# Kernel optimization log

Hardware: AMD Instinct MI355X
Metric: run time of the kernel (lower is better)

## Reference

```python
import jax, jax.numpy as jnp
import numpy as np

FPS_RATIO = 0.1
K = 20
EPS = 1e-6
COS_EPS = 1e-8  # torch nn.CosineSimilarity default eps


def setup_inputs() -> dict:
    key = jax.random.key(0)
    k1, k2 = jax.random.split(key)
    N = 40000
    pos = jax.random.normal(k1, (N, 3), dtype=jnp.float32) * 10.0   # spatial coordinates
    vec_pred = jax.random.normal(k2, (N, 3), dtype=jnp.float32)     # predicted direction vectors
    return {"vec_pred": vec_pred, "pos": pos}


def _fps(pos, n_anchors):
    """Deterministic farthest point sampling starting from point 0. Returns [n_anchors] int32."""
    d0 = jnp.sum((pos - pos[0]) ** 2, axis=-1)  # [N]
    def body(min_d, _):
        idx = jnp.argmax(min_d)
        d = jnp.sum((pos - pos[idx]) ** 2, axis=-1)
        return jnp.minimum(min_d, d), idx.astype(jnp.int32)
    _, idxs = jax.lax.scan(body, d0, None, length=n_anchors - 1)
    return jnp.concatenate([jnp.zeros((1,), jnp.int32), idxs])


def _vec_loss(vec_pred, pos):
    N = pos.shape[0]
    n_anchors = int(np.ceil(FPS_RATIO * N))
    anchors = _fps(pos, n_anchors)
    anchors_pos = pos[anchors]                                     # [A, 3]
    # Brute-force KNN: squared distances anchors -> all points, [A, N]
    d2 = (jnp.sum(anchors_pos ** 2, -1, keepdims=True)
          - 2.0 * anchors_pos @ pos.T
          + jnp.sum(pos ** 2, -1)[None, :])
    _, nn_idx = jax.lax.top_k(-d2, K)                              # [A, K]
    nbhds = pos[nn_idx]                                            # [A, K, 3]
    # pca_lowrank: center then SVD; principal direction = top right singular vector
    centered = nbhds - jnp.mean(nbhds, axis=1, keepdims=True)
    _, _, vh = jnp.linalg.svd(centered, full_matrices=False)       # vh: [A, 3, 3]
    vecs = vh[:, 0, :]                                             # [A, 3]
    # Faithful to original: index[0] (anchor ids, each repeated K times) indexes BOTH tensors
    idx0 = jnp.repeat(jnp.arange(n_anchors), K)                    # [A*K]
    a = vec_pred[idx0]
    b = vecs[idx0]
    denom = (jnp.maximum(jnp.linalg.norm(a, axis=-1), COS_EPS)
             * jnp.maximum(jnp.linalg.norm(b, axis=-1), COS_EPS))
    abs_cos = jnp.abs(jnp.sum(a * b, axis=-1) / denom)
    return -jnp.mean(jnp.log(abs_cos + EPS))


def reference(vec_pred, pos):
    # single graph -> forward's average over graphs is just this scalar
    return _vec_loss(vec_pred, pos)
```

## Files before the change

### kernel.cpp

```cpp
#include <hip/hip_runtime.h>
#include <math.h>

#define N_PTS       40000
#define N_ANCH      4000
#define KNN         20
#define NFB         128
#define BT          64
#define NWAVES      128
#define STRIDE      (NWAVES * 64)
#define PPT         5
#define TW          4
#define POOL        (NWAVES * TW)
#define RSLOTS      (POOL / 64)
#define CCAP        6

typedef unsigned long long ull;

#define LD_RLX(p)    __hip_atomic_load((p),  __ATOMIC_RELAXED, __HIP_MEMORY_SCOPE_AGENT)
#define ST_REL(p,v)  __hip_atomic_store((p), (v), __ATOMIC_RELEASE, __HIP_MEMORY_SCOPE_AGENT)
#define ST_RLX(p,v)  __hip_atomic_store((p), (v), __ATOMIC_RELAXED, __HIP_MEMORY_SCOPE_AGENT)


__device__ __forceinline__ double dist64(double px, double py, double pz,
                                         double wx, double wy, double wz) {
  double dx = px - wx, dy = py - wy, dz = pz - wz;
  return dx * dx + dy * dy + dz * dz;
}

__device__ __forceinline__ unsigned key32(double v) {
  unsigned hi = (unsigned)__double2hiint(v);
  return (hi & 0x80000000u) ? ~hi : (hi | 0x80000000u);
}

__device__ __forceinline__ ull pack_key(double v, int idx) {
  ull b = (ull)__double_as_longlong(v);
  ull m = (b >> 63) ? ~b : (b | 0x8000000000000000ull);
  return (m & 0xFFFFFFFFFFFF0000ull) | ((ull)(0xFFFF - idx) & 0xFFFFull);
}

__device__ __forceinline__ unsigned wave_umax_dpp(unsigned x) {
#define DPP_STEP(ctrl) { unsigned y = (unsigned)__builtin_amdgcn_update_dpp( \
      0, (int)x, ctrl, 0xf, 0xf, true); x = (y > x) ? y : x; }
  DPP_STEP(0x111)
  DPP_STEP(0x112)
  DPP_STEP(0x114)
  DPP_STEP(0x118)
  DPP_STEP(0x142)
  DPP_STEP(0x143)
#undef DPP_STEP
  return (unsigned)__builtin_amdgcn_readlane((int)x, 63);
}

__device__ __forceinline__ int rl_i(int v, int l) { return __builtin_amdgcn_readlane(v, l); }
__device__ __forceinline__ double rl_d(double v, int l) {
  int lo = __builtin_amdgcn_readlane(__double2loint(v), l);
  int hi = __builtin_amdgcn_readlane(__double2hiint(v), l);
  return __hiloint2double(hi, lo);
}
__device__ __forceinline__ ull rl_u64(ull v, int l) {
  int lo = __builtin_amdgcn_readlane((int)(unsigned)(v & 0xffffffffull), l);
  int hi = __builtin_amdgcn_readlane((int)(unsigned)(v >> 32), l);
  return ((ull)(unsigned)hi << 32) | (unsigned)lo;
}

__device__ __forceinline__ void wave_argmax_exact(double& wv, int& wix) {
#pragma unroll
  for (int off = 1; off < 64; off <<= 1) {
    double ov = __shfl_xor(wv, off);
    int    oi = __shfl_xor(wix, off);
    bool bt = (ov > wv) || (ov == wv && oi < wix);
    wv = bt ? ov : wv; wix = bt ? oi : wix;
  }
}

__device__ __forceinline__ void wave_pick(double v, int idx,
                                          unsigned& wkey, int& wlane, int& widx) {
  unsigned k = key32(v);
  unsigned M = wave_umax_dpp(k);
  ull mask = __ballot(k == M);
  if (__popcll(mask) == 1) {
    wlane = __ffsll(mask) - 1;
    widx  = rl_i(idx, wlane);
    wkey  = M;
  } else {
    double wv = v; int wi = idx;
    wave_argmax_exact(wv, wi);
    widx = wi;
    wkey = key32(wv);
    ull m2 = __ballot(idx == widx);
    wlane = __ffsll(m2) - 1;
  }
}

struct FpsSm {
  ull    lv[CCAP * 64];
  float  lc[CCAP * 64][3];
};
struct KnnSm { int w[KNN]; };
union Smem { FpsSm f; KnnSm k; };

__device__ static inline void eig3_maxvec(double xx, double xy, double xz,
                                          double yy, double yz, double zz,
                                          double& v0, double& v1, double& v2) {
  double q  = (xx + yy + zz) / 3.0;
  double p1 = xy * xy + xz * xz + yz * yz;
  double a00 = xx - q, a11 = yy - q, a22 = zz - q;
  double p2 = a00 * a00 + a11 * a11 + a22 * a22 + 2.0 * p1;
  if (p2 < 1e-300) { v0 = 1.0; v1 = 0.0; v2 = 0.0; return; }
  double p   = sqrt(p2 / 6.0);
  double inv = 1.0 / p;
  double b00 = a00 * inv, b01 = xy * inv, b02 = xz * inv;
  double b11 = a11 * inv, b12 = yz * inv, b22 = a22 * inv;
  double detB = b00 * (b11 * b22 - b12 * b12)
              - b01 * (b01 * b22 - b12 * b02)
              + b02 * (b01 * b12 - b11 * b02);
  double r = fmin(1.0, fmax(-1.0, detB * 0.5));
  double phi = acos(r) / 3.0;
  double lam = q + 2.0 * p * cos(phi);

  double r0x = xx - lam, r0y = xy,       r0z = xz;
  double r1x = xy,       r1y = yy - lam, r1z = yz;
  double r2x = xz,       r2y = yz,       r2z = zz - lam;
  double c0x = r0y * r1z - r0z * r1y, c0y = r0z * r1x - r0x * r1z, c0z = r0x * r1y - r0y * r1x;
  double c1x = r0y * r2z - r0z * r2y, c1y = r0z * r2x - r0x * r2z, c1z = r0x * r2y - r0y * r2x;
  double c2x = r1y * r2z - r1z * r2y, c2y = r1z * r2x - r1x * r2z, c2z = r1x * r2y - r1y * r2x;
  double n0 = c0x * c0x + c0y * c0y + c0z * c0z;
  double n1 = c1x * c1x + c1y * c1y + c1z * c1z;
  double n2 = c2x * c2x + c2y * c2y + c2z * c2z;
  double bx = c0x, by = c0y, bz = c0z, bn = n0;
  if (n1 > bn) { bx = c1x; by = c1y; bz = c1z; bn = n1; }
  if (n2 > bn) { bx = c2x; by = c2y; bz = c2z; bn = n2; }
  if (bn < 1e-280) { v0 = 1.0; v1 = 0.0; v2 = 0.0; return; }
  double s = 1.0 / sqrt(bn);
  v0 = bx * s; v1 = by * s; v2 = bz * s;
}

__global__ __launch_bounds__(BT, 2) void fps_knn_kernel(
    const float* __restrict__ pos, const float* __restrict__ vec_pred,
    int* __restrict__ flag, ull* __restrict__ slots,
    int* __restrict__ anchors, double* __restrict__ acc) {
  __shared__ Smem sm;
  const int lane = threadIdx.x & 63;

  if (blockIdx.x < NFB) {
    __builtin_amdgcn_s_setprio(1);

    const int gw   = blockIdx.x;
    const int gtid = gw * 64 + lane;

    double pdx[PPT], pdy[PPT], pdz[PPT], md[PPT];
    const double a0x = (double)pos[0], a0y = (double)pos[1], a0z = (double)pos[2];
#pragma unroll
    for (int k = 0; k < PPT; ++k) {
      int i = gtid + k * STRIDE;
      if (i < N_PTS) {
        pdx[k] = (double)pos[3 * i];
        pdy[k] = (double)pos[3 * i + 1];
        pdz[k] = (double)pos[3 * i + 2];
        md[k]  = dist64(pdx[k], pdy[k], pdz[k], a0x, a0y, a0z);
      } else {
        pdx[k] = 0.0; pdy[k] = 0.0; pdz[k] = 0.0;
        md[k]  = -1.0e300;
      }
    }
    if (gw == 0 && lane == 0) ST_RLX(anchors + 0, 0);

    double bv = -1.0e301; int bi = 0x7fffffff;
#pragma unroll
    for (int k = 0; k < PPT; ++k) {
      int i = gtid + k * STRIDE;
      bool bt = (md[k] > bv) || (md[k] == bv && i < bi);
      bv = bt ? md[k] : bv; bi = bt ? i : bi;
    }

    int nsel  = 1;
    int batch = 0;
#pragma unroll 1
    while (nsel < N_ANCH) {
      batch++;
      const int par = batch & 1;

      unsigned cons = 0;
      double pv = -1.0e301; int pix = 0;
#pragma unroll 1
      for (int r = 0; r < TW; ++r) {
        unsigned wkey; int wlane, widx;
        wave_pick(bv, bi, wkey, wlane, widx);
        double wval = rl_d(bv, wlane);
        if (lane == wlane && bi != 0x7fffffff) {
          cons |= 1u << ((unsigned)(bi - gtid) >> 13);
          bv = -1.0e301; bi = 0x7fffffff;
#pragma unroll
          for (int k = 0; k < PPT; ++k) {
            if (!((cons >> k) & 1u)) {
              int i = gtid + k * STRIDE;
              bool bt = (md[k] > bv) || (md[k] == bv && i < bi);
              bv = bt ? md[k] : bv; bi = bt ? i : bi;
            }
          }
        }
        if (lane == r) { pv = wval; pix = widx; }
      }

      if (lane < TW) {
        ST_RLX(&slots[par * POOL + gw * TW + lane], pack_key(pv, pix));
      }
      if (lane == 0) ST_REL(flag + gw, batch);

      for (;;) {
        int f0 = LD_RLX(flag + lane);
        int f1 = LD_RLX(flag + 64 + lane);
        if (__ballot((f0 >= batch) && (f1 >= batch)) == ~0ull) break;
        __builtin_amdgcn_s_sleep(1);
      }
      __builtin_amdgcn_sched_barrier(0);

      ull pk[RSLOTS];
#pragma unroll
      for (int j = 0; j < RSLOTS; ++j)
        pk[j] = LD_RLX(&slots[par * POOL + lane + 64 * j]);

      unsigned kj[RSLOTS];
      unsigned lkmax = 0;
#pragma unroll
      for (int j = 0; j < RSLOTS; ++j) {
        kj[j] = (unsigned)(pk[j] >> 32);
        lkmax = (kj[j] > lkmax) ? kj[j] : lkmax;
      }
      const unsigned Mkey    = wave_umax_dpp(lkmax);
      const unsigned BmaxKey = wave_umax_dpp(((lane & 3) == 3) ? lkmax : 0u);

      int cap = N_ANCH - nsel;
      int S = 0;

      if (Mkey > BmaxKey) {
        int base = 0;
#pragma unroll
        for (int j = 0; j < RSLOTS; ++j) {
          bool live = kj[j] > BmaxKey;
          ull bal = __ballot(live);
          int rank = base + (int)__popcll(bal & ((1ull << lane) - 1ull));
          if (live) {
            sm.f.lv[rank] = pk[j];
            int p = 0xFFFF - (int)(pk[j] & 0xFFFFull);
            sm.f.lc[rank][0] = pos[3 * p];
            sm.f.lc[rank][1] = pos[3 * p + 1];
            sm.f.lc[rank][2] = pos[3 * p + 2];
          }
          base += (int)__popcll(bal);
        }
        const int live_n = base;

        ull pk2[CCAP]; double c2x[CCAP], c2y[CCAP], c2z[CCAP];
#pragma unroll
        for (int tt = 0; tt < CCAP; ++tt) {
          if (live_n > tt * 64) {
            int e = tt * 64 + lane;
            bool ok = e < live_n;
            ull    v  = sm.f.lv[e];
            float  x  = sm.f.lc[e][0];
            float  y  = sm.f.lc[e][1];
            float  z  = sm.f.lc[e][2];
            pk2[tt] = ok ? v : 0ull;
            c2x[tt] = ok ? (double)x : 0.0;
            c2y[tt] = ok ? (double)y : 0.0;
            c2z[tt] = ok ? (double)z : 0.0;
          } else {
            pk2[tt] = 0ull;
            c2x[tt] = 0.0; c2y[tt] = 0.0; c2z[tt] = 0.0;
          }
        }

#pragma unroll 1
        while (S < cap) {
          ull pa, pb, pc, wpk; double ax_, ay_, az_, bx_, by_, bz_, fx, fy, fz;
          { bool t = pk2[1] > pk2[0];
            pa = t ? pk2[1] : pk2[0];
            ax_ = t ? c2x[1] : c2x[0]; ay_ = t ? c2y[1] : c2y[0]; az_ = t ? c2z[1] : c2z[0]; }
          { bool t = pk2[3] > pk2[2];
            pb = t ? pk2[3] : pk2[2];
            bx_ = t ? c2x[3] : c2x[2]; by_ = t ? c2y[3] : c2y[2]; bz_ = t ? c2z[3] : c2z[2]; }
          { bool t = pk2[5] > pk2[4];
            pc = t ? pk2[5] : pk2[4];
            fx = t ? c2x[5] : c2x[4]; fy = t ? c2y[5] : c2y[4]; fz = t ? c2z[5] : c2z[4]; }
          { bool t = pb > pa;
            pa = t ? pb : pa;
            ax_ = t ? bx_ : ax_; ay_ = t ? by_ : ay_; az_ = t ? bz_ : az_; }
          { bool t = pc > pa;
            wpk = t ? pc : pa;
            fx = t ? fx : ax_; fy = t ? fy : ay_; fz = t ? fz : az_; }

          unsigned k = (unsigned)(wpk >> 32);
          unsigned M = wave_umax_dpp(k);
          ull mask = __ballot(k == M);
          ull full; int wlane;
          if (__popcll(mask) == 1) {
            wlane = __ffsll(mask) - 1;
            full  = rl_u64(wpk, wlane);
          } else {
            ull g = wpk;
#pragma unroll
            for (int off = 1; off < 64; off <<= 1) {
              ull o = __shfl_xor(g, off);
              g = (o > g) ? o : g;
            }
            full = g;
            ull m2 = __ballot(wpk == full);
            wlane = __ffsll(m2) - 1;
          }
          unsigned wkey = (unsigned)(full >> 32);
          if (S != 0 && !(wkey > BmaxKey)) break;
          int widx = 0xFFFF - (int)(full & 0xFFFFull);
          double wxd = rl_d(fx, wlane), wyd = rl_d(fy, wlane), wzd = rl_d(fz, wlane);
          if (gw == 0 && lane == 0) ST_RLX(anchors + nsel + S, widx);

#pragma unroll
          for (int tt = 0; tt < CCAP; ++tt) {
            if (live_n > tt * 64) {
              double d = dist64(c2x[tt], c2y[tt], c2z[tt], wxd, wyd, wzd);
              ull db  = (ull)__double_as_longlong(d);
              ull dpk = ((db | 0x8000000000000000ull) & 0xFFFFFFFFFFFF0000ull)
                      | (pk2[tt] & 0xFFFFull);
              ull nv  = (dpk < pk2[tt]) ? dpk : pk2[tt];
              pk2[tt] = (pk2[tt] == full) ? 0ull : nv;
            }
          }
#pragma unroll
          for (int k2 = 0; k2 < PPT; ++k2)
            md[k2] = fmin(md[k2], dist64(pdx[k2], pdy[k2], pdz[k2], wxd, wyd, wzd));
          S++;
        }
      } else {
#pragma unroll 1
        while (S < cap) {
          ull wpk = pk[0];
#pragma unroll
          for (int j = 1; j < RSLOTS; ++j) wpk = (pk[j] > wpk) ? pk[j] : wpk;
          ull g = wpk;
#pragma unroll
          for (int off = 1; off < 64; off <<= 1) {
            ull o = __shfl_xor(g, off);
            g = (o > g) ? o : g;
          }
          unsigned wkey = (unsigned)(g >> 32);
          if (S != 0 && !(wkey > BmaxKey)) break;
          int widx = 0xFFFF - (int)(g & 0xFFFFull);
          if (widx < 0) widx = 0;
          if (widx >= N_PTS) widx = N_PTS - 1;
          double wxd = (double)pos[3 * widx];
          double wyd = (double)pos[3 * widx + 1];
          double wzd = (double)pos[3 * widx + 2];
          if (gw == 0 && lane == 0) ST_RLX(anchors + nsel + S, widx);
#pragma unroll
          for (int j = 0; j < RSLOTS; ++j) {
            int p = 0xFFFF - (int)(pk[j] & 0xFFFFull);
            if (p < 0) p = 0;
            if (p >= N_PTS) p = N_PTS - 1;
            double d = dist64((double)pos[3 * p], (double)pos[3 * p + 1],
                              (double)pos[3 * p + 2], wxd, wyd, wzd);
            ull db  = (ull)__double_as_longlong(d);
            ull dpk = ((db | 0x8000000000000000ull) & 0xFFFFFFFFFFFF0000ull)
                    | (pk[j] & 0xFFFFull);
            ull nv  = (dpk < pk[j]) ? dpk : pk[j];
            pk[j] = (pk[j] == g) ? 0ull : nv;
          }
#pragma unroll
          for (int k2 = 0; k2 < PPT; ++k2)
            md[k2] = fmin(md[k2], dist64(pdx[k2], pdy[k2], pdz[k2], wxd, wyd, wzd));
          S++;
        }
      }
      nsel += S;

      bv = -1.0e301; bi = 0x7fffffff;
#pragma unroll
      for (int k = 0; k < PPT; ++k) {
        int i = gtid + k * STRIDE;
        bool bt = (md[k] > bv) || (md[k] == bv && i < bi);
        bv = bt ? md[k] : bv; bi = bt ? i : bi;
      }
    }
  } else {
    const int aidx = blockIdx.x - NFB;
    int a = -1;
    for (;;) {
      if (lane == 0) a = LD_RLX(anchors + aidx);
      a = __shfl(a, 0);
      if (a >= 0) break;
      __builtin_amdgcn_s_sleep(32);
    }
    const int ai = a;
    const float ax = pos[3 * ai], ay = pos[3 * ai + 1], az = pos[3 * ai + 2];

    ull key[KNN];
#pragma unroll
    for (int s = 0; s < KNN; ++s) key[s] = ~0ull;
    ull kmax = ~0ull; int smax = 0;
#pragma unroll 1
    for (int k = 0; k < N_PTS / 64; ++k) {
      int j = (k << 6) + lane;
      float dx = pos[3 * j] - ax, dy = pos[3 * j + 1] - ay, dz = pos[3 * j + 2] - az;
      float d  = dx * dx + dy * dy + dz * dz;
      ull nk = ((ull)__float_as_uint(d) << 32) | (unsigned)j;
      if (nk < kmax) {
#pragma unroll
        for (int s = 0; s < KNN; ++s) key[s] = (s == smax) ? nk : key[s];
        kmax = 0ull; smax = 0;
#pragma unroll
        for (int s = 0; s < KNN; ++s) {
          bool g = key[s] > kmax;
          kmax = g ? key[s] : kmax;
          smax = g ? s : smax;
        }
      }
    }

    ull lmin = ~0ull; int ls = 0;
#pragma unroll
    for (int s = 0; s < KNN; ++s) {
      bool l = key[s] < lmin;
      lmin = l ? key[s] : lmin; ls = l ? s : ls;
    }
#pragma unroll 1
    for (int r = 0; r < KNN; ++r) {
      ull g = lmin;
#pragma unroll
      for (int off = 1; off < 64; off <<= 1) {
        ull ov = __shfl_xor(g, off);
        g = (ov < g) ? ov : g;
      }
      if (lane == 0) sm.k.w[r] = (int)(g & 0xffffffffull);
      if (lmin == g) {
#pragma unroll
        for (int s = 0; s < KNN; ++s) key[s] = (s == ls) ? ~0ull : key[s];
        lmin = ~0ull; ls = 0;
#pragma unroll
        for (int s = 0; s < KNN; ++s) {
          bool l = key[s] < lmin;
          lmin = l ? key[s] : lmin; ls = l ? s : ls;
        }
      }
    }

    if (lane == 0) {
      double mx = 0, my = 0, mz = 0;
      for (int r = 0; r < KNN; ++r) {
        int p = sm.k.w[r];
        mx += (double)pos[3 * p]; my += (double)pos[3 * p + 1]; mz += (double)pos[3 * p + 2];
      }
      mx /= KNN; my /= KNN; mz /= KNN;
      double xx = 0, xy = 0, xz = 0, yy = 0, yz = 0, zz = 0;
      for (int r = 0; r < KNN; ++r) {
        int p = sm.k.w[r];
        double cx = (double)pos[3 * p]     - mx;
        double cy = (double)pos[3 * p + 1] - my;
        double cz = (double)pos[3 * p + 2] - mz;
        xx += cx * cx; xy += cx * cy; xz += cx * cz;
        yy += cy * cy; yz += cy * cz; zz += cz * cz;
      }
      double v0, v1, v2;
      eig3_maxvec(xx, xy, xz, yy, yz, zz, v0, v1, v2);

      double a0 = vec_pred[3 * aidx], a1 = vec_pred[3 * aidx + 1], a2 = vec_pred[3 * aidx + 2];
      double an = sqrt(a0 * a0 + a1 * a1 + a2 * a2);
      double bn = sqrt(v0 * v0 + v1 * v1 + v2 * v2);
      double denom = fmax(an, 1e-8) * fmax(bn, 1e-8);
      double c = fabs((a0 * v0 + a1 * v1 + a2 * v2) / denom);
      atomicAdd(acc, log(c + 1e-6));
    }
  }
}

__global__ void finalize_kernel(const double* __restrict__ acc, float* __restrict__ out) {
  out[0] = (float)(-acc[0] / (double)N_ANCH);
}

extern "C" void kernel_launch(void* const* d_in, const int* in_sizes, int n_in,
                              void* d_out, int out_size, void* d_ws, size_t ws_size,
                              hipStream_t stream) {
  (void)in_sizes; (void)n_in; (void)out_size; (void)ws_size;
  const float* vec_pred = (const float*)d_in[0];
  const float* pos      = (const float*)d_in[1];
  float* out = (float*)d_out;

  char* ws = (char*)d_ws;
  double* acc     = (double*)(ws + 0);
  int*    flag    = (int*)(ws + 64);
  ull*    slots   = (ull*)(ws + 1024);
  int*    anchors = (int*)(ws + 17408);

  hipMemsetAsync(ws, 0, 1024, stream);
  hipMemsetAsync(ws + 17408, 0xFF, N_ANCH * 4, stream);
  hipLaunchKernelGGL(fps_knn_kernel, dim3(NFB + N_ANCH), dim3(BT), 0, stream,
                     pos, vec_pred, flag, slots, anchors, acc);
  hipLaunchKernelGGL(finalize_kernel, dim3(1), dim3(1), 0, stream, acc, out);
}
```

Before: 3.092 ms.

## Replace per-wave flag barrier with batch-tagged slots and widen per-wave candidate pool

The separate flag array used for cross-block synchronization is removed. Each published slot now carries an 8-bit batch tag, so consumers spin on the slot data itself, which removes one release store and a separate polling round-trip per batch. Each wave also publishes 8 candidates instead of 4, so more anchors can be selected per global sync round. Candidate coordinates are kept in float registers instead of double. The cost is that 8 fewer bits of the distance key are kept for ordering, and the candidate arrays are larger, which raises register pressure.

```diff
diff --git a/kernel.cpp b/kernel.cpp
--- a/kernel.cpp
+++ b/kernel.cpp
@@ -9,17 +9,19 @@
 #define NWAVES      128
 #define STRIDE      (NWAVES * 64)
 #define PPT         5
-#define TW          4
+#define TW          8
 #define POOL        (NWAVES * TW)
 #define RSLOTS      (POOL / 64)
-#define CCAP        6
+#define CCAP        14
 
 typedef unsigned long long ull;
 
 #define LD_RLX(p)    __hip_atomic_load((p),  __ATOMIC_RELAXED, __HIP_MEMORY_SCOPE_AGENT)
-#define ST_REL(p,v)  __hip_atomic_store((p), (v), __ATOMIC_RELEASE, __HIP_MEMORY_SCOPE_AGENT)
 #define ST_RLX(p,v)  __hip_atomic_store((p), (v), __ATOMIC_RELAXED, __HIP_MEMORY_SCOPE_AGENT)
 
+
+#define VMASK 0xFFFFFFFFFF000000ull
+#define TMASK 0x0000000000FF0000ull
 
 __device__ __forceinline__ double dist64(double px, double py, double pz,
                                          double wx, double wy, double wz) {
@@ -32,10 +34,11 @@
   return (hi & 0x80000000u) ? ~hi : (hi | 0x80000000u);
 }
 
-__device__ __forceinline__ ull pack_key(double v, int idx) {
+__device__ __forceinline__ ull pack_pub(double v, int idx, int batch) {
   ull b = (ull)__double_as_longlong(v);
   ull m = (b >> 63) ? ~b : (b | 0x8000000000000000ull);
-  return (m & 0xFFFFFFFFFFFF0000ull) | ((ull)(0xFFFF - idx) & 0xFFFFull);
+  return (m & VMASK) | (((ull)(batch & 0xFF)) << 16)
+       | ((ull)(0xFFFF - idx) & 0xFFFFull);
 }
 
 __device__ __forceinline__ unsigned wave_umax_dpp(unsigned x) {
@@ -52,6 +55,9 @@
 }
 
 __device__ __forceinline__ int rl_i(int v, int l) { return __builtin_amdgcn_readlane(v, l); }
+__device__ __forceinline__ float rl_f(float v, int l) {
+  return __int_as_float(__builtin_amdgcn_readlane(__float_as_int(v), l));
+}
 __device__ __forceinline__ double rl_d(double v, int l) {
   int lo = __builtin_amdgcn_readlane(__double2loint(v), l);
   int hi = __builtin_amdgcn_readlane(__double2hiint(v), l);
@@ -141,6 +147,7 @@
     int* __restrict__ anchors, double* __restrict__ acc) {
   __shared__ Smem sm;
   const int lane = threadIdx.x & 63;
+  (void)flag;
 
   if (blockIdx.x < NFB) {
     __builtin_amdgcn_s_setprio(1);
@@ -179,6 +186,7 @@
     while (nsel < N_ANCH) {
       batch++;
       const int par = batch & 1;
+      const unsigned tag8 = (unsigned)(batch & 0xFF);
 
       unsigned cons = 0;
       double pv = -1.0e301; int pix = 0;
@@ -203,22 +211,23 @@
       }
 
       if (lane < TW) {
-        ST_RLX(&slots[par * POOL + gw * TW + lane], pack_key(pv, pix));
-      }
-      if (lane == 0) ST_REL(flag + gw, batch);
-
+        ST_RLX(&slots[par * POOL + gw * TW + lane], pack_pub(pv, pix, batch));
+      }
+
+      ull pk[RSLOTS];
       for (;;) {
-        int f0 = LD_RLX(flag + lane);
-        int f1 = LD_RLX(flag + 64 + lane);
-        if (__ballot((f0 >= batch) && (f1 >= batch)) == ~0ull) break;
+        bool ok = true;
+#pragma unroll
+        for (int j = 0; j < RSLOTS; ++j) {
+          pk[j] = LD_RLX(&slots[par * POOL + lane + 64 * j]);
+          ok &= (((unsigned)(pk[j] >> 16) & 0xFFu) == tag8);
+        }
+        if (__ballot(ok) == ~0ull) break;
         __builtin_amdgcn_s_sleep(1);
       }
       __builtin_amdgcn_sched_barrier(0);
-
-      ull pk[RSLOTS];
-#pragma unroll
-      for (int j = 0; j < RSLOTS; ++j)
-        pk[j] = LD_RLX(&slots[par * POOL + lane + 64 * j]);
+#pragma unroll
+      for (int j = 0; j < RSLOTS; ++j) pk[j] &= ~TMASK;
 
       unsigned kj[RSLOTS];
       unsigned lkmax = 0;
@@ -228,7 +237,7 @@
         lkmax = (kj[j] > lkmax) ? kj[j] : lkmax;
       }
       const unsigned Mkey    = wave_umax_dpp(lkmax);
-      const unsigned BmaxKey = wave_umax_dpp(((lane & 3) == 3) ? lkmax : 0u);
+      const unsigned BmaxKey = wave_umax_dpp(((lane & 7) == 7) ? lkmax : 0u);
 
       int cap = N_ANCH - nsel;
       int S = 0;
@@ -251,7 +260,7 @@
         }
         const int live_n = base;
 
-        ull pk2[CCAP]; double c2x[CCAP], c2y[CCAP], c2z[CCAP];
+        ull pk2[CCAP]; float c2x[CCAP], c2y[CCAP], c2z[CCAP];
 #pragma unroll
         for (int tt = 0; tt < CCAP; ++tt) {
           if (live_n > tt * 64) {
@@ -262,33 +271,26 @@
             float  y  = sm.f.lc[e][1];
             float  z  = sm.f.lc[e][2];
             pk2[tt] = ok ? v : 0ull;
-            c2x[tt] = ok ? (double)x : 0.0;
-            c2y[tt] = ok ? (double)y : 0.0;
-            c2z[tt] = ok ? (double)z : 0.0;
+            c2x[tt] = ok ? x : 0.0f;
+            c2y[tt] = ok ? y : 0.0f;
+            c2z[tt] = ok ? z : 0.0f;
           } else {
             pk2[tt] = 0ull;
-            c2x[tt] = 0.0; c2y[tt] = 0.0; c2z[tt] = 0.0;
+            c2x[tt] = 0.0f; c2y[tt] = 0.0f; c2z[tt] = 0.0f;
           }
         }
 
 #pragma unroll 1
         while (S < cap) {
-          ull pa, pb, pc, wpk; double ax_, ay_, az_, bx_, by_, bz_, fx, fy, fz;
-          { bool t = pk2[1] > pk2[0];
-            pa = t ? pk2[1] : pk2[0];
-            ax_ = t ? c2x[1] : c2x[0]; ay_ = t ? c2y[1] : c2y[0]; az_ = t ? c2z[1] : c2z[0]; }
-          { bool t = pk2[3] > pk2[2];
-            pb = t ? pk2[3] : pk2[2];
-            bx_ = t ? c2x[3] : c2x[2]; by_ = t ? c2y[3] : c2y[2]; bz_ = t ? c2z[3] : c2z[2]; }
-          { bool t = pk2[5] > pk2[4];
-            pc = t ? pk2[5] : pk2[4];
-            fx = t ? c2x[5] : c2x[4]; fy = t ? c2y[5] : c2y[4]; fz = t ? c2z[5] : c2z[4]; }
-          { bool t = pb > pa;
-            pa = t ? pb : pa;
-            ax_ = t ? bx_ : ax_; ay_ = t ? by_ : ay_; az_ = t ? bz_ : az_; }
-          { bool t = pc > pa;
-            wpk = t ? pc : pa;
-            fx = t ? fx : ax_; fy = t ? fy : ay_; fz = t ? fz : az_; }
+          ull wpk = pk2[0]; float fx = c2x[0], fy = c2y[0], fz = c2z[0];
+#pragma unroll
+          for (int tt = 1; tt < CCAP; ++tt) {
+            if (live_n > tt * 64) {
+              bool t = pk2[tt] > wpk;
+              wpk = t ? pk2[tt] : wpk;
+              fx = t ? c2x[tt] : fx; fy = t ? c2y[tt] : fy; fz = t ? c2z[tt] : fz;
+            }
+          }
 
           unsigned k = (unsigned)(wpk >> 32);
           unsigned M = wave_umax_dpp(k);
@@ -311,15 +313,18 @@
           unsigned wkey = (unsigned)(full >> 32);
           if (S != 0 && !(wkey > BmaxKey)) break;
           int widx = 0xFFFF - (int)(full & 0xFFFFull);
-          double wxd = rl_d(fx, wlane), wyd = rl_d(fy, wlane), wzd = rl_d(fz, wlane);
+          double wxd = (double)rl_f(fx, wlane);
+          double wyd = (double)rl_f(fy, wlane);
+          double wzd = (double)rl_f(fz, wlane);
           if (gw == 0 && lane == 0) ST_RLX(anchors + nsel + S, widx);
 
 #pragma unroll
           for (int tt = 0; tt < CCAP; ++tt) {
             if (live_n > tt * 64) {
-              double d = dist64(c2x[tt], c2y[tt], c2z[tt], wxd, wyd, wzd);
+              double d = dist64((double)c2x[tt], (double)c2y[tt], (double)c2z[tt],
+                                wxd, wyd, wzd);
               ull db  = (ull)__double_as_longlong(d);
-              ull dpk = ((db | 0x8000000000000000ull) & 0xFFFFFFFFFFFF0000ull)
+              ull dpk = ((db | 0x8000000000000000ull) & VMASK)
                       | (pk2[tt] & 0xFFFFull);
               ull nv  = (dpk < pk2[tt]) ? dpk : pk2[tt];
               pk2[tt] = (pk2[tt] == full) ? 0ull : nv;
@@ -359,7 +364,7 @@
             double d = dist64((double)pos[3 * p], (double)pos[3 * p + 1],
                               (double)pos[3 * p + 2], wxd, wyd, wzd);
             ull db  = (ull)__double_as_longlong(d);
-            ull dpk = ((db | 0x8000000000000000ull) & 0xFFFFFFFFFFFF0000ull)
+            ull dpk = ((db | 0x8000000000000000ull) & VMASK)
                     | (pk[j] & 0xFFFFull);
             ull nv  = (dpk < pk[j]) ? dpk : pk[j];
             pk[j] = (pk[j] == g) ? 0ull : nv;
@@ -489,7 +494,7 @@
   ull*    slots   = (ull*)(ws + 1024);
   int*    anchors = (int*)(ws + 17408);
 
-  hipMemsetAsync(ws, 0, 1024, stream);
+  hipMemsetAsync(ws, 0, 17408, stream);
   hipMemsetAsync(ws + 17408, 0xFF, N_ANCH * 4, stream);
   hipLaunchKernelGGL(fps_knn_kernel, dim3(NFB + N_ANCH), dim3(BT), 0, stream,
                      pos, vec_pred, flag, slots, anchors, acc);
```

Result: slower. 4.256 ms (+37.6%).
